# Performance work log

Hardware: AMD Instinct MI355X
Metric: run time of the kernel (lower is better)

## Reference

```python
import jax, jax.numpy as jnp
import numpy as np

N, E, D, H, L, NEF = 50000, 500000, 128, 4, 4, 7
Dh = D // H
LN_EPS = 1e-5


def layer_norm(x, g, b):
    mu = x.mean(-1, keepdims=True)
    var = ((x - mu) ** 2).mean(-1, keepdims=True)
    return (x - mu) / jnp.sqrt(var + LN_EPS) * g + b


def setup_inputs() -> dict:
    key = jax.random.key(0)
    ks = iter(jax.random.split(key, 64))
    p = lambda shape, s=0.05: jax.random.normal(next(ks), shape, dtype=jnp.float32) * s
    inp = {
        'x_nodes': jnp.zeros((N,), dtype=jnp.int32),
        'edge_index': jax.random.randint(next(ks), (2, E), 0, N, dtype=jnp.int32),
        'edge_attr': p((E, NEF), 1.0),
        'node_table': p((1, D), 1.0),
        'Wee': p((NEF, D)), 'bee': jnp.zeros((D,), jnp.float32),
        'Wq': p((L, D, D)), 'bq': jnp.zeros((L, D), jnp.float32),
        'Wk': p((L, D, D)), 'bk': jnp.zeros((L, D), jnp.float32),
        'Wv': p((L, D, D)), 'bv': jnp.zeros((L, D), jnp.float32),
        'We': p((L, D, D)), 'be': jnp.zeros((L, D), jnp.float32),
        'Ws': p((L, D, D)), 'bs': jnp.zeros((L, D), jnp.float32),
        'W1': p((L, D, 2 * D)), 'b1': jnp.zeros((L, 2 * D), jnp.float32),
        'W2': p((L, 2 * D, D)), 'b2': jnp.zeros((L, D), jnp.float32),
        'n1g': jnp.ones((L, D), jnp.float32), 'n1b': jnp.zeros((L, D), jnp.float32),
        'n2g': jnp.ones((L, D), jnp.float32), 'n2b': jnp.zeros((L, D), jnp.float32),
        'lng': jnp.ones((L, D), jnp.float32), 'lnb': jnp.zeros((L, D), jnp.float32),
    }
    return inp


def reference(x_nodes, edge_index, edge_attr, node_table, Wee, bee,
              Wq, bq, Wk, bk, Wv, bv, We, be, Ws, bs,
              W1, b1, W2, b2, n1g, n1b, n2g, n2b, lng, lnb):
    src, dst = edge_index[0], edge_index[1]
    scale = 1.0 / np.sqrt(Dh).astype(np.float32)
    # node encoder: Embedding(1, D) with indices clamped to [0, 0]
    h = node_table[jnp.clip(x_nodes, 0, 0)]              # [N, D]
    ee = edge_attr @ Wee + bee                            # [E, D]
    for l in range(L):
        h_in = h
        # TransformerConv (PyG semantics, root_weight=True, eval mode)
        q = (h_in @ Wq[l] + bq[l]).reshape(N, H, Dh)
        k = (h_in @ Wk[l] + bk[l]).reshape(N, H, Dh)
        v = (h_in @ Wv[l] + bv[l]).reshape(N, H, Dh)
        e = (ee @ We[l] + be[l]).reshape(E, H, Dh)
        ke = k[src] + e                                   # [E, H, Dh]
        ve = v[src] + e                                   # [E, H, Dh]
        alpha = (q[dst] * ke).sum(-1) * scale             # [E, H]
        m = jax.ops.segment_max(alpha, dst, num_segments=N)
        m = jnp.where(jnp.isfinite(m), m, 0.0)
        ex = jnp.exp(alpha - m[dst])
        den = jax.ops.segment_sum(ex, dst, num_segments=N) + 1e-16
        attn = ex / den[dst]                              # [E, H]
        agg = jax.ops.segment_sum(attn[:, :, None] * ve, dst, num_segments=N)
        att_out = agg.reshape(N, D) + (h_in @ Ws[l] + bs[l])  # skip (root) term
        # transformer block: residual + LN, FFN + residual + LN
        x1 = layer_norm(h_in + att_out, n1g[l], n1b[l])
        ff = jax.nn.leaky_relu(x1 @ W1[l] + b1[l]) @ W2[l] + b2[l]
        hconv = layer_norm(x1 + ff, n2g[l], n2b[l])
        # outer per-layer LayerNorm + activation (except last) + residual
        hn = layer_norm(hconv, lng[l], lnb[l])
        if l < L - 1:
            hn = jax.nn.leaky_relu(hn)
        h = hn + h_in
    return h  # JK == 'last'
```

## Files before the change

kernel.cpp:

```cpp
#include <hip/hip_runtime.h>
#include <hip/hip_bf16.h>
#include <math.h>

#define N_NODES 50000
#define N_EDGES 500000
#define DIM     128
#define NLAYER  4
#define NEFEAT  7

static constexpr float LN_EPS    = 1e-5f;
static constexpr float ATT_SCALE = 0.17677669529663687f;

typedef short s16x8 __attribute__((ext_vector_type(8)));
typedef float f32x4 __attribute__((ext_vector_type(4)));

static __device__ __forceinline__ float leaky(float x){ return x >= 0.f ? x : 0.01f*x; }

static __device__ __forceinline__ unsigned short f2bf(float f){
    __hip_bfloat16 b = __float2bfloat16(f);
    return *reinterpret_cast<unsigned short*>(&b);
}
static __device__ __forceinline__ float bflo(unsigned int u){ return __uint_as_float(u << 16); }
static __device__ __forceinline__ float bfhi(unsigned int u){ return __uint_as_float(u & 0xFFFF0000u); }

template<int CTRL>
static __device__ __forceinline__ float dpp_ror_add(float x){
    int r = __builtin_amdgcn_update_dpp(0, __float_as_int(x), CTRL, 0xf, 0xf, true);
    return x + __int_as_float(r);
}
static __device__ __forceinline__ float sum16(float x){
    x = dpp_ror_add<0x128>(x);
    x = dpp_ror_add<0x124>(x);
    x = dpp_ror_add<0x122>(x);
    x = dpp_ror_add<0x121>(x);
    return x;
}
static __device__ __forceinline__ float sum64(float x){
    x = sum16(x);
    x += __shfl_xor(x, 16);
    x += __shfl_xor(x, 32);
    return x;
}

__global__ void init_h_kernel(const float* __restrict__ node_table,
                              float* __restrict__ h, unsigned short* __restrict__ hb){
    int i = blockIdx.x*blockDim.x + threadIdx.x;
    if (i < N_NODES*DIM){
        float v = node_table[i & (DIM-1)];
        h[i]  = v;
        hb[i] = f2bf(v);
    }
}

__global__ void zero2_kernel(int* __restrict__ a, int* __restrict__ b){
    int i = blockIdx.x*blockDim.x + threadIdx.x;
    if (i < N_NODES){ a[i] = 0; b[i] = 0; }
}

__global__ void count_kernel(const int* __restrict__ dst, int* __restrict__ cnt){
    int e = blockIdx.x*blockDim.x + threadIdx.x;
    if (e < N_EDGES) atomicAdd(&cnt[dst[e]], 1);
}

__global__ void scan_kernel(const int* __restrict__ cnt, int* __restrict__ rowptr){
    __shared__ int wsum[16];
    __shared__ int runsh;
    if (threadIdx.x == 0) runsh = 0;
    __syncthreads();
    int lane = threadIdx.x & 63, wid = threadIdx.x >> 6;
    for (int base = 0; base < N_NODES; base += 1024){
        int i = base + (int)threadIdx.x;
        int vv = (i < N_NODES) ? cnt[i] : 0;
        int s = vv;
        #pragma unroll
        for (int off = 1; off < 64; off <<= 1){
            int t = __shfl_up(s, off);
            if (lane >= off) s += t;
        }
        if (lane == 63) wsum[wid] = s;
        __syncthreads();
        if (wid == 0 && lane < 16){
            int x = wsum[lane];
            #pragma unroll
            for (int off = 1; off < 16; off <<= 1){
                int t = __shfl_up(x, off);
                if (lane >= off) x += t;
            }
            wsum[lane] = x;
        }
        __syncthreads();
        int wpre = (wid == 0) ? 0 : wsum[wid-1];
        int run  = runsh;
        if (i < N_NODES) rowptr[i] = run + wpre + s - vv;
        __syncthreads();
        if (threadIdx.x == 0) runsh = run + wsum[15];
        __syncthreads();
    }
    if (threadIdx.x == 0) rowptr[N_NODES] = runsh;
}

__global__ void scatter_kernel(const int* __restrict__ src, const int* __restrict__ dst,
                               const float* __restrict__ edge_attr,
                               const int* __restrict__ rowptr, int* __restrict__ fill,
                               int* __restrict__ srcs, unsigned int* __restrict__ eab){
    int e = blockIdx.x*blockDim.x + threadIdx.x;
    if (e >= N_EDGES) return;
    int d   = dst[e];
    int pos = rowptr[d] + atomicAdd(&fill[d], 1);
    srcs[pos] = src[e];
    const float* a = edge_attr + (size_t)e*NEFEAT;
    uint4 u;
    u.x = (unsigned int)f2bf(a[0]) | ((unsigned int)f2bf(a[1]) << 16);
    u.y = (unsigned int)f2bf(a[2]) | ((unsigned int)f2bf(a[3]) << 16);
    u.z = (unsigned int)f2bf(a[4]) | ((unsigned int)f2bf(a[5]) << 16);
    u.w = (unsigned int)f2bf(a[6]) | (0x3F80u << 16);
    *(uint4*)(eab + (size_t)pos*4) = u;
}

__global__ void weff_all_kernel(const float* __restrict__ Wee, const float* __restrict__ bee,
                                const float* __restrict__ We, const float* __restrict__ be,
                                float* __restrict__ weff){
    int l = blockIdx.x;
    int d = threadIdx.x;
    const float* We_l = We + (size_t)l*DIM*DIM;
    float* out = weff + (size_t)l*8*DIM;
    for (int c = 0; c < NEFEAT; ++c){
        float s = 0.f;
        for (int t = 0; t < DIM; ++t) s += Wee[c*DIM + t] * We_l[t*DIM + d];
        out[c*DIM + d] = s;
    }
    float s = 0.f;
    for (int t = 0; t < DIM; ++t) s += bee[t] * We_l[t*DIM + d];
    out[7*DIM + d] = s + be[l*DIM + d];
}

__global__ void prepw_kernel(const float* __restrict__ Wq, const float* __restrict__ Wk,
                             const float* __restrict__ Wv, const float* __restrict__ Ws,
                             const float* __restrict__ W1, const float* __restrict__ W2,
                             unsigned short* __restrict__ wqkvsT,
                             unsigned short* __restrict__ w1T,
                             unsigned short* __restrict__ w2T){
    int tid = blockIdx.x*blockDim.x + threadIdx.x;
    if (tid >= NLAYER*131072) return;
    int l = tid >> 17;
    int r = tid & 131071;
    if (r < 65536){
        int n = r >> 7, k = r & 127;
        int p = n >> 7, nn = n & 127;
        const float* W = (p==0)?Wq:(p==1)?Wk:(p==2)?Wv:Ws;
        float val = W[(size_t)l*DIM*DIM + (size_t)k*DIM + nn];
        wqkvsT[(size_t)l*65536 + (size_t)n*128 + k] = f2bf(val);
    } else if (r < 98304){
        int r2 = r - 65536;
        int n = r2 >> 7, k = r2 & 127;
        float val = W1[(size_t)l*32768 + (size_t)k*256 + n];
        w1T[(size_t)l*32768 + (size_t)n*128 + k] = f2bf(val);
    } else {
        int r2 = r - 98304;
        int n = r2 >> 8, k = r2 & 255;
        float val = W2[(size_t)l*32768 + (size_t)k*128 + n];
        w2T[(size_t)l*32768 + (size_t)n*256 + k] = f2bf(val);
    }
}

__global__ __launch_bounds__(256) void qkvs_mfma_kernel(
    const unsigned short* __restrict__ hb, const unsigned short* __restrict__ wT,
    const float* __restrict__ bq, const float* __restrict__ bk,
    const float* __restrict__ bv, const float* __restrict__ bs,
    unsigned int* __restrict__ qs, unsigned int* __restrict__ kv)
{
    __shared__ char sA[32*256];
    int row0 = blockIdx.x*32;
    for (int idx = threadIdx.x; idx < 512; idx += 256){
        int row = idx >> 4, k16 = idx & 15;
        int byte = row*256 + k16*16;  byte ^= (row & 7) << 4;
        s16x8 val = {0,0,0,0,0,0,0,0};
        int grow = row0 + row;
        if (grow < N_NODES) val = *(const s16x8*)(hb + (size_t)grow*128 + k16*8);
        *(s16x8*)(sA + byte) = val;
    }
    __syncthreads();

    int w = threadIdx.x >> 6, l = threadIdx.x & 63;
    int y = blockIdx.y;
    int pb0 = y ? 128 : 0;
    int pb1 = y ? 256 : 384;

    f32x4 acc[2][4];
    #pragma unroll
    for (int rf=0;rf<2;++rf)
        #pragma unroll
        for (int cf=0;cf<4;++cf) acc[rf][cf] = (f32x4){0.f,0.f,0.f,0.f};

    s16x8 af[2][2], bf[2][4];
    #pragma unroll
    for (int rf=0;rf<2;++rf){
        int row = rf*16 + (l & 15);
        int byte = row*256 + (l >> 4)*16;  byte ^= (row & 7) << 4;
        af[0][rf] = *(const s16x8*)(sA + byte);
    }
    #pragma unroll
    for (int cf=0;cf<4;++cf){
        int nrow = ((cf < 2) ? pb0 : pb1) + (w<<5) + ((cf&1)<<4) + (l & 15);
        bf[0][cf] = *(const s16x8*)(wT + (size_t)nrow*128 + (l >> 4)*8);
    }
    #pragma unroll
    for (int kb = 0; kb < 4; ++kb){
        int cur = kb & 1, nxt = cur ^ 1;
        if (kb < 3){
            #pragma unroll
            for (int rf=0;rf<2;++rf){
                int row = rf*16 + (l & 15);
                int byte = row*256 + (kb+1)*64 + (l >> 4)*16;  byte ^= (row & 7) << 4;
                af[nxt][rf] = *(const s16x8*)(sA + byte);
            }
            #pragma unroll
            for (int cf=0;cf<4;++cf){
                int nrow = ((cf < 2) ? pb0 : pb1) + (w<<5) + ((cf&1)<<4) + (l & 15);
                bf[nxt][cf] = *(const s16x8*)(wT + (size_t)nrow*128 + (kb+1)*32 + (l >> 4)*8);
            }
        }
        #pragma unroll
        for (int rf=0;rf<2;++rf)
            #pragma unroll
            for (int cf=0;cf<4;++cf)
                acc[rf][cf] = __builtin_amdgcn_mfma_f32_16x16x32_bf16(af[cur][rf], bf[cur][cf], acc[rf][cf], 0, 0, 0);
    }

    const float* biasLo = y ? bk : bq;
    const float* biasHi = y ? bv : bs;
    unsigned int* outp  = y ? kv : qs;
    #pragma unroll
    for (int cp = 0; cp < 2; ++cp){
        int col = (w<<5) + (cp<<4) + (l & 15);
        float blo = biasLo[col], bhi = biasHi[col];
        #pragma unroll
        for (int rf=0;rf<2;++rf){
            #pragma unroll
            for (int r=0;r<4;++r){
                int row = row0 + rf*16 + ((l >> 4) << 2) + r;
                if (row < N_NODES){
                    float lo = acc[rf][cp][r]   + blo;
                    float hi = acc[rf][cp+2][r] + bhi;
                    outp[(size_t)row*128 + col] =
                        (unsigned int)f2bf(lo) | ((unsigned int)f2bf(hi) << 16);
                }
            }
        }
    }
}

__global__ __launch_bounds__(256) void attn_kernel(
    const unsigned int* __restrict__ qs, const unsigned int* __restrict__ kv,
    const float* __restrict__ weff_l, const int* __restrict__ rowptr,
    const int* __restrict__ srcs, const unsigned int* __restrict__ eab,
    const float* __restrict__ h,
    const float* __restrict__ n1g, const float* __restrict__ n1b,
    unsigned short* __restrict__ x1b)
{
    __shared__ float wf[8][DIM];
    __shared__ float els[4][64][9];
    for (int i = threadIdx.x; i < 8*DIM; i += 256) ((float*)wf)[i] = weff_l[i];
    __syncthreads();
    int wv = threadIdx.x >> 6, lane = threadIdx.x & 63;
    int n = blockIdx.x*4 + wv;
    if (n >= N_NODES) return;
    float (*el)[9] = els[wv];

    int d0 = lane*2;
    int fi = lane & 15;
    int fc = fi & 7;

    uint2 qsb = *(const uint2*)(qs + (size_t)n*DIM + d0);
    float q0 = bflo(qsb.x)*ATT_SCALE, q1 = bflo(qsb.y)*ATT_SCALE;
    float s0 = bfhi(qsb.x), s1 = bfhi(qsb.y);

    float qe[8];
    #pragma unroll
    for (int c = 0; c < 8; ++c){
        float2 wc = *(const float2*)&wf[c][d0];
        qe[c] = sum16(q0*wc.x + q1*wc.y);
    }
    float qaug = qe[0];
    qaug = (fc==1) ? qe[1] : qaug;
    qaug = (fc==2) ? qe[2] : qaug;
    qaug = (fc==3) ? qe[3] : qaug;
    qaug = (fc==4) ? qe[4] : qaug;
    qaug = (fc==5) ? qe[5] : qaug;
    qaug = (fc==6) ? qe[6] : qaug;
    qaug = (fc==7) ? qe[7] : qaug;
    qaug = (fi < 8) ? qaug : 0.f;

    int beg = rowptr[n], deg = rowptr[n+1] - beg;
    float a0 = 0.f, a1 = 0.f, peaL = 0.f;

    for (int cb = 0; cb < deg; cb += 64){
        int base = beg + cb;
        int cdeg = deg - cb; if (cdeg > 64) cdeg = 64;
        int srcv = 0;
        uint4 eu = {0u,0u,0u,0u};
        if (cb + lane < deg){
            srcv = srcs[base + lane];
            eu = *(const uint4*)(eab + ((size_t)(base + lane) << 2));
        }
        asm volatile("s_waitcnt lgkmcnt(0)" ::: "memory");
        __builtin_amdgcn_sched_barrier(0);
        {
            float* row = el[lane];
            row[0] = bflo(eu.x); row[1] = bfhi(eu.x);
            row[2] = bflo(eu.y); row[3] = bfhi(eu.y);
            row[4] = bflo(eu.z); row[5] = bfhi(eu.z);
            row[6] = bflo(eu.w); row[7] = bfhi(eu.w);
        }
        asm volatile("s_waitcnt lgkmcnt(0)" ::: "memory");
        __builtin_amdgcn_sched_barrier(0);

        int j = 0;
        for (; j + 1 < cdeg; j += 2){
            int svA = __builtin_amdgcn_readlane(srcv, j);
            int svB = __builtin_amdgcn_readlane(srcv, j+1);
            uint2 kvA = *(const uint2*)(kv + (size_t)svA*DIM + d0);
            uint2 kvB = *(const uint2*)(kv + (size_t)svB*DIM + d0);
            float eaA = el[j][fc];
            float eaB = el[j+1][fc];
            float pA = sum16(q0*bflo(kvA.x) + q1*bflo(kvA.y) + qaug*eaA);
            float pB = sum16(q0*bflo(kvB.x) + q1*bflo(kvB.y) + qaug*eaB);
            float ppA = __expf(pA);
            float ppB = __expf(pB);
            a0   += ppA*bfhi(kvA.x) + ppB*bfhi(kvB.x);
            a1   += ppA*bfhi(kvA.y) + ppB*bfhi(kvB.y);
            peaL += ppA*eaA + ppB*eaB;
        }
        if (j < cdeg){
            int sv = __builtin_amdgcn_readlane(srcv, j);
            uint2 kva = *(const uint2*)(kv + (size_t)sv*DIM + d0);
            float ea = el[j][fc];
            float p = sum16(q0*bflo(kva.x) + q1*bflo(kva.y) + qaug*ea);
            float pp = __expf(p);
            a0   += pp*bfhi(kva.x);
            a1   += pp*bfhi(kva.y);
            peaL += pp*ea;
        }
    }

    int hb_ = lane & 48;
    float pc0 = __shfl(peaL, hb_ + 0);
    float pc1 = __shfl(peaL, hb_ + 1);
    float pc2 = __shfl(peaL, hb_ + 2);
    float pc3 = __shfl(peaL, hb_ + 3);
    float pc4 = __shfl(peaL, hb_ + 4);
    float pc5 = __shfl(peaL, hb_ + 5);
    float pc6 = __shfl(peaL, hb_ + 6);
    float den = __shfl(peaL, hb_ + 7);

    float inv = (den > 0.f) ? 1.f/den : 0.f;
    float ev0, ev1;
    {
        float2 w0 = *(const float2*)&wf[0][d0];
        float2 w1c = *(const float2*)&wf[1][d0];
        float2 w2c = *(const float2*)&wf[2][d0];
        float2 w3c = *(const float2*)&wf[3][d0];
        float2 w4c = *(const float2*)&wf[4][d0];
        float2 w5c = *(const float2*)&wf[5][d0];
        float2 w6c = *(const float2*)&wf[6][d0];
        float2 w7c = *(const float2*)&wf[7][d0];
        ev0 = pc0*w0.x + pc1*w1c.x + pc2*w2c.x + pc3*w3c.x
            + pc4*w4c.x + pc5*w5c.x + pc6*w6c.x + den*w7c.x;
        ev1 = pc0*w0.y + pc1*w1c.y + pc2*w2c.y + pc3*w3c.y
            + pc4*w4c.y + pc5*w5c.y + pc6*w6c.y + den*w7c.y;
    }

    float2 hv = *(const float2*)(h + (size_t)n*DIM + d0);
    float t0 = hv.x + (a0 + ev0)*inv + s0;
    float t1 = hv.y + (a1 + ev1)*inv + s1;
    float sum = sum64(t0 + t1);
    float ss  = sum64(t0*t0 + t1*t1);
    float mu = sum * (1.f/DIM);
    float rstd = rsqrtf(ss*(1.f/DIM) - mu*mu + LN_EPS);
    float o0 = (t0-mu)*rstd*n1g[d0]   + n1b[d0];
    float o1 = (t1-mu)*rstd*n1g[d0+1] + n1b[d0+1];
    unsigned int pk = (unsigned int)f2bf(o0) | ((unsigned int)f2bf(o1) << 16);
    *(unsigned int*)(x1b + (size_t)n*DIM + d0) = pk;
}

__global__ __launch_bounds__(256) void ffn_mfma_kernel(
    const unsigned short* __restrict__ x1b,
    const float* __restrict__ hin,
    const unsigned short* __restrict__ w1T, const float* __restrict__ b1,
    const unsigned short* __restrict__ w2T, const float* __restrict__ b2,
    const float* __restrict__ n2g, const float* __restrict__ n2b,
    const float* __restrict__ lng, const float* __restrict__ lnb,
    int apply_act, float* __restrict__ h, unsigned short* __restrict__ hb)
{
    __shared__ char smem[24576];
    char* sA   = smem;
    char* sMid = smem + 8192;
    int row0 = blockIdx.x*32;
    for (int idx = threadIdx.x; idx < 512; idx += 256){
        int row = idx >> 4, k16 = idx & 15;
        int byte = row*256 + k16*16;  byte ^= (row & 7) << 4;
        s16x8 val = {0,0,0,0,0,0,0,0};
        int grow = row0 + row;
        if (grow < N_NODES) val = *(const s16x8*)(x1b + (size_t)grow*128 + k16*8);
        *(s16x8*)(sA + byte) = val;
    }
    __syncthreads();

    int w = threadIdx.x >> 6, l = threadIdx.x & 63;

    {
        int n0 = w*64;
        f32x4 acc[2][4];
        #pragma unroll
        for (int rf=0;rf<2;++rf)
            #pragma unroll
            for (int cf=0;cf<4;++cf) acc[rf][cf] = (f32x4){0.f,0.f,0.f,0.f};
        s16x8 af[2][2], bfr[2][4];
        #pragma unroll
        for (int rf=0;rf<2;++rf){
            int row = rf*16 + (l & 15);
            int byte = row*256 + (l >> 4)*16;  byte ^= (row & 7) << 4;
            af[0][rf] = *(const s16x8*)(sA + byte);
        }
        #pragma unroll
        for (int cf=0;cf<4;++cf){
            int n = n0 + cf*16 + (l & 15);
            bfr[0][cf] = *(const s16x8*)(w1T + (size_t)n*128 + (l >> 4)*8);
        }
        #pragma unroll
        for (int kb = 0; kb < 4; ++kb){
            int cur = kb & 1, nxt = cur ^ 1;
            if (kb < 3){
                #pragma unroll
                for (int rf=0;rf<2;++rf){
                    int row = rf*16 + (l & 15);
                    int byte = row*256 + (kb+1)*64 + (l >> 4)*16;  byte ^= (row & 7) << 4;
                    af[nxt][rf] = *(const s16x8*)(sA + byte);
                }
                #pragma unroll
                for (int cf=0;cf<4;++cf){
                    int n = n0 + cf*16 + (l & 15);
                    bfr[nxt][cf] = *(const s16x8*)(w1T + (size_t)n*128 + (kb+1)*32 + (l >> 4)*8);
                }
            }
            #pragma unroll
            for (int rf=0;rf<2;++rf)
                #pragma unroll
                for (int cf=0;cf<4;++cf)
                    acc[rf][cf] = __builtin_amdgcn_mfma_f32_16x16x32_bf16(af[cur][rf], bfr[cur][cf], acc[rf][cf], 0, 0, 0);
        }
        #pragma unroll
        for (int cf=0;cf<4;++cf){
            int col = n0 + cf*16 + (l & 15);
            float bb = b1[col];
            #pragma unroll
            for (int rf=0;rf<2;++rf){
                #pragma unroll
                for (int r=0;r<4;++r){
                    int row = rf*16 + ((l >> 4) << 2) + r;
                    float val = leaky(acc[rf][cf][r] + bb);
                    int byte = row*512 + col*2;  byte ^= (row & 7) << 4;
                    *(unsigned short*)(sMid + byte) = f2bf(val);
                }
            }
        }
    }
    __syncthreads();

    f32x4 acc2[2][2];
    {
        int n0 = w*32;
        #pragma unroll
        for (int cf=0;cf<2;++cf)
            #pragma unroll
            for (int rf=0;rf<2;++rf) acc2[cf][rf] = (f32x4){0.f,0.f,0.f,0.f};
        s16x8 af[2][2], bfr[2][2];
        #pragma unroll
        for (int rf=0;rf<2;++rf){
            int row = rf*16 + (l & 15);
            int byte = row*512 + (l >> 4)*16;  byte ^= (row & 7) << 4;
            af[0][rf] = *(const s16x8*)(sMid + byte);
        }
        #pragma unroll
        for (int cf=0;cf<2;++cf){
            int n = n0 + cf*16 + (l & 15);
            bfr[0][cf] = *(const s16x8*)(w2T + (size_t)n*256 + (l >> 4)*8);
        }
        #pragma unroll
        for (int kb = 0; kb < 8; ++kb){
            int cur = kb & 1, nxt = cur ^ 1;
            if (kb < 7){
                #pragma unroll
                for (int rf=0;rf<2;++rf){
                    int row = rf*16 + (l & 15);
                    int byte = row*512 + (kb+1)*64 + (l >> 4)*16;  byte ^= (row & 7) << 4;
                    af[nxt][rf] = *(const s16x8*)(sMid + byte);
                }
                #pragma unroll
                for (int cf=0;cf<2;++cf){
                    int n = n0 + cf*16 + (l & 15);
                    bfr[nxt][cf] = *(const s16x8*)(w2T + (size_t)n*256 + (kb+1)*32 + (l >> 4)*8);
                }
            }
            #pragma unroll
            for (int cf=0;cf<2;++cf)
                #pragma unroll
                for (int rf=0;rf<2;++rf)
                    acc2[cf][rf] = __builtin_amdgcn_mfma_f32_16x16x32_bf16(af[cur][rf], bfr[cur][cf], acc2[cf][rf], 0, 0, 0);
        }
    }
    __syncthreads();

    float* sFF = (float*)sMid;
    {
        int n0 = w*32;
        #pragma unroll
        for (int cf=0;cf<2;++cf){
            int col = n0 + cf*16 + (l & 15);
            float bb = b2[col];
            #pragma unroll
            for (int rf=0;rf<2;++rf){
                #pragma unroll
                for (int r=0;r<4;++r){
                    int row = rf*16 + ((l >> 4) << 2) + r;
                    int byte = row*512 + col*4;  byte ^= (row & 7) << 4;
                    *(float*)((char*)sFF + byte) = acc2[cf][rf][r] + bb;
                }
            }
        }
    }
    __syncthreads();

    int d0 = l*2;
    float g2a = n2g[d0], g2b = n2g[d0+1], be2a = n2b[d0], be2b = n2b[d0+1];
    float gla = lng[d0], glb = lng[d0+1], bla = lnb[d0], blb = lnb[d0+1];
    for (int i = 0; i < 8; ++i){
        int rr = w*8 + i;
        int grow = row0 + rr;
        if (grow >= N_NODES) break;
        int byte = rr*512 + d0*4;  byte ^= (rr & 7) << 4;
        float2 ff = *(float2*)((char*)sFF + byte);
        int byteA = rr*256 + d0*2;  byteA ^= (rr & 7) << 4;
        unsigned int xu = *(unsigned int*)(sA + byteA);
        float2 hr = *(const float2*)(hin + (size_t)grow*DIM + d0);
        float t0 = bflo(xu) + ff.x, t1 = bfhi(xu) + ff.y;
        float sum = sum64(t0 + t1);
        float ss  = sum64(t0*t0 + t1*t1);
        float mu = sum*(1.f/DIM);
        float rstd = rsqrtf(ss*(1.f/DIM) - mu*mu + LN_EPS);
        float c0 = (t0-mu)*rstd*g2a + be2a;
        float c1 = (t1-mu)*rstd*g2b + be2b;
        float sum2 = sum64(c0 + c1);
        float ss2  = sum64(c0*c0 + c1*c1);
        float mu2 = sum2*(1.f/DIM);
        float rstd2 = rsqrtf(ss2*(1.f/DIM) - mu2*mu2 + LN_EPS);
        float z0 = (c0-mu2)*rstd2*gla + bla;
        float z1 = (c1-mu2)*rstd2*glb + blb;
        if (apply_act){ z0 = leaky(z0); z1 = leaky(z1); }
        float o0 = z0 + hr.x, o1 = z1 + hr.y;
        *(float2*)(h + (size_t)grow*DIM + d0) = make_float2(o0, o1);
        unsigned int pk = (unsigned int)f2bf(o0) | ((unsigned int)f2bf(o1) << 16);
        *(unsigned int*)(hb + (size_t)grow*DIM + d0) = pk;
    }
}

extern "C" void kernel_launch(void* const* d_in, const int* in_sizes, int n_in,
                              void* d_out, int out_size, void* d_ws, size_t ws_size,
                              hipStream_t stream)
{
    const int*   edge_index = (const int*)  d_in[1];
    const float* edge_attr  = (const float*)d_in[2];
    const float* node_table = (const float*)d_in[3];
    const float* Wee = (const float*)d_in[4];
    const float* bee = (const float*)d_in[5];
    const float* Wq  = (const float*)d_in[6];  const float* bq = (const float*)d_in[7];
    const float* Wk  = (const float*)d_in[8];  const float* bk = (const float*)d_in[9];
    const float* Wv  = (const float*)d_in[10]; const float* bv = (const float*)d_in[11];
    const float* We  = (const float*)d_in[12]; const float* be = (const float*)d_in[13];
    const float* Ws  = (const float*)d_in[14]; const float* bs = (const float*)d_in[15];
    const float* W1  = (const float*)d_in[16]; const float* b1 = (const float*)d_in[17];
    const float* W2  = (const float*)d_in[18]; const float* b2 = (const float*)d_in[19];
    const float* n1g = (const float*)d_in[20]; const float* n1b = (const float*)d_in[21];
    const float* n2g = (const float*)d_in[22]; const float* n2b = (const float*)d_in[23];
    const float* lng = (const float*)d_in[24]; const float* lnb = (const float*)d_in[25];

    float* h = (float*)d_out;

    char* ws = (char*)d_ws;
    size_t off = 0;
    auto alloc = [&](size_t bytes)->void*{
        void* p = ws + off;
        off += (bytes + 255) & ~(size_t)255;
        return p;
    };
    unsigned int*   qs   = (unsigned int*)  alloc(sizeof(int)*(size_t)N_NODES*DIM);
    unsigned int*   kv   = (unsigned int*)  alloc(sizeof(int)*(size_t)N_NODES*DIM);
    unsigned short* hb   = (unsigned short*)alloc(sizeof(short)*(size_t)N_NODES*DIM);
    unsigned short* x1b  = (unsigned short*)alloc(sizeof(short)*(size_t)N_NODES*DIM);
    unsigned int*   eab  = (unsigned int*)  alloc(sizeof(int)*(size_t)N_EDGES*4);
    unsigned short* wqkvsT = (unsigned short*)alloc(sizeof(short)*NLAYER*512*128);
    unsigned short* w1T    = (unsigned short*)alloc(sizeof(short)*NLAYER*256*128);
    unsigned short* w2T    = (unsigned short*)alloc(sizeof(short)*NLAYER*128*256);
    float* weff = (float*)alloc(sizeof(float)*NLAYER*8*DIM);
    int* rowptr = (int*)alloc(sizeof(int)*(N_NODES+1));
    int* cnt    = (int*)alloc(sizeof(int)*N_NODES);
    int* fill   = (int*)alloc(sizeof(int)*N_NODES);
    int* srcs   = (int*)alloc(sizeof(int)*N_EDGES);

    const int* srcIdx = edge_index;
    const int* dstIdx = edge_index + N_EDGES;

    init_h_kernel<<<(N_NODES*DIM+255)/256, 256, 0, stream>>>(node_table, h, hb);
    zero2_kernel<<<(N_NODES+255)/256, 256, 0, stream>>>(cnt, fill);
    count_kernel<<<(N_EDGES+255)/256, 256, 0, stream>>>(dstIdx, cnt);
    scan_kernel<<<1, 1024, 0, stream>>>(cnt, rowptr);
    scatter_kernel<<<(N_EDGES+255)/256, 256, 0, stream>>>(srcIdx, dstIdx, edge_attr,
                                                          rowptr, fill, srcs, eab);
    prepw_kernel<<<(NLAYER*131072+255)/256, 256, 0, stream>>>(Wq, Wk, Wv, Ws, W1, W2,
                                                              wqkvsT, w1T, w2T);
    weff_all_kernel<<<NLAYER, 128, 0, stream>>>(Wee, bee, We, be, weff);

    int tiles32 = (N_NODES + 31)/32;
    for (int l = 0; l < NLAYER; ++l){
        qkvs_mfma_kernel<<<dim3(tiles32, 2), 256, 0, stream>>>(hb,
            wqkvsT + (size_t)l*65536,
            bq + (size_t)l*DIM, bk + (size_t)l*DIM, bv + (size_t)l*DIM, bs + (size_t)l*DIM,
            qs, kv);
        attn_kernel<<<(N_NODES+3)/4, 256, 0, stream>>>(qs, kv,
            weff + (size_t)l*8*DIM, rowptr, srcs, eab, h,
            n1g + (size_t)l*DIM, n1b + (size_t)l*DIM, x1b);
        ffn_mfma_kernel<<<tiles32, 256, 0, stream>>>(x1b, h,
            w1T + (size_t)l*32768, b1 + (size_t)l*2*DIM,
            w2T + (size_t)l*32768, b2 + (size_t)l*DIM,
            n2g + (size_t)l*DIM, n2b + (size_t)l*DIM,
            lng + (size_t)l*DIM, lnb + (size_t)l*DIM,
            (l < NLAYER-1) ? 1 : 0, h, hb);
    }
}
```

Measured before the change: 662.9 us.

## Fuse next-layer QKVS projection into FFN kernel and parallelize CSR scan

The FFN kernel now keeps the new bf16 hidden rows in shared memory and computes the next layer's Q/K/V/S projection directly, dropping the separate qkvs kernel launches and the hb round trip through global memory for layers after the first. The single-block serial prefix scan is replaced with a three-kernel block scan. Residual loads are hoisted ahead of the LayerNorm loop. In exchange, each FFN block does more work (64 output columns per wave, two passes), which adds register pressure, and the FFN grid has half as many blocks as the old 2D qkvs grid.

```diff
diff --git a/kernel.cpp b/kernel.cpp
--- a/kernel.cpp
+++ b/kernel.cpp
@@ -62,41 +62,53 @@
     if (e < N_EDGES) atomicAdd(&cnt[dst[e]], 1);
 }
 
-__global__ void scan_kernel(const int* __restrict__ cnt, int* __restrict__ rowptr){
+__global__ void scan1_kernel(const int* __restrict__ cnt, int* __restrict__ rowptr,
+                             int* __restrict__ bsum){
     __shared__ int wsum[16];
-    __shared__ int runsh;
-    if (threadIdx.x == 0) runsh = 0;
-    __syncthreads();
-    int lane = threadIdx.x & 63, wid = threadIdx.x >> 6;
-    for (int base = 0; base < N_NODES; base += 1024){
-        int i = base + (int)threadIdx.x;
-        int vv = (i < N_NODES) ? cnt[i] : 0;
-        int s = vv;
-        #pragma unroll
-        for (int off = 1; off < 64; off <<= 1){
-            int t = __shfl_up(s, off);
-            if (lane >= off) s += t;
-        }
-        if (lane == 63) wsum[wid] = s;
-        __syncthreads();
-        if (wid == 0 && lane < 16){
-            int x = wsum[lane];
-            #pragma unroll
-            for (int off = 1; off < 16; off <<= 1){
-                int t = __shfl_up(x, off);
-                if (lane >= off) x += t;
-            }
-            wsum[lane] = x;
-        }
-        __syncthreads();
-        int wpre = (wid == 0) ? 0 : wsum[wid-1];
-        int run  = runsh;
-        if (i < N_NODES) rowptr[i] = run + wpre + s - vv;
-        __syncthreads();
-        if (threadIdx.x == 0) runsh = run + wsum[15];
-        __syncthreads();
-    }
-    if (threadIdx.x == 0) rowptr[N_NODES] = runsh;
+    int t = threadIdx.x;
+    int i = blockIdx.x*1024 + t;
+    int lane = t & 63, wid = t >> 6;
+    int v = (i < N_NODES) ? cnt[i] : 0;
+    int s = v;
+    #pragma unroll
+    for (int off = 1; off < 64; off <<= 1){
+        int tt = __shfl_up(s, off);
+        if (lane >= off) s += tt;
+    }
+    if (lane == 63) wsum[wid] = s;
+    __syncthreads();
+    if (wid == 0 && lane < 16){
+        int x = wsum[lane];
+        #pragma unroll
+        for (int off = 1; off < 16; off <<= 1){
+            int tt = __shfl_up(x, off);
+            if (lane >= off) x += tt;
+        }
+        wsum[lane] = x;
+    }
+    __syncthreads();
+    int wpre = (wid == 0) ? 0 : wsum[wid-1];
+    if (i < N_NODES) rowptr[i] = wpre + s - v;
+    if (t == 1023) bsum[blockIdx.x] = wpre + s;
+}
+
+__global__ void scan2_kernel(const int* __restrict__ bsum, int* __restrict__ boff,
+                             int nb, int* __restrict__ totalp){
+    int t = threadIdx.x;
+    int v = (t < nb) ? bsum[t] : 0;
+    int s = v;
+    #pragma unroll
+    for (int off = 1; off < 64; off <<= 1){
+        int tt = __shfl_up(s, off);
+        if (t >= off) s += tt;
+    }
+    if (t < nb) boff[t] = s - v;
+    if (t == 63) *totalp = s;
+}
+
+__global__ void scan3_kernel(int* __restrict__ rowptr, const int* __restrict__ boff){
+    int i = blockIdx.x*1024 + threadIdx.x;
+    if (i < N_NODES) rowptr[i] += boff[blockIdx.x];
 }
 
 __global__ void scatter_kernel(const int* __restrict__ src, const int* __restrict__ dst,
@@ -383,14 +395,18 @@
     *(unsigned int*)(x1b + (size_t)n*DIM + d0) = pk;
 }
 
-__global__ __launch_bounds__(256) void ffn_mfma_kernel(
+__global__ __launch_bounds__(256) void ffn_qkvs_kernel(
     const unsigned short* __restrict__ x1b,
     const float* __restrict__ hin,
     const unsigned short* __restrict__ w1T, const float* __restrict__ b1,
     const unsigned short* __restrict__ w2T, const float* __restrict__ b2,
     const float* __restrict__ n2g, const float* __restrict__ n2b,
     const float* __restrict__ lng, const float* __restrict__ lnb,
-    int apply_act, float* __restrict__ h, unsigned short* __restrict__ hb)
+    int apply_act, float* __restrict__ h,
+    int do_qkvs, const unsigned short* __restrict__ wTn,
+    const float* __restrict__ bqn, const float* __restrict__ bkn,
+    const float* __restrict__ bvn, const float* __restrict__ bsn,
+    unsigned int* __restrict__ qs, unsigned int* __restrict__ kv)
 {
     __shared__ char smem[24576];
     char* sA   = smem;
@@ -534,6 +550,14 @@
     int d0 = l*2;
     float g2a = n2g[d0], g2b = n2g[d0+1], be2a = n2b[d0], be2b = n2b[d0+1];
     float gla = lng[d0], glb = lng[d0+1], bla = lnb[d0], blb = lnb[d0+1];
+    float2 hrv[8];
+    #pragma unroll
+    for (int i = 0; i < 8; ++i){
+        int grow = row0 + w*8 + i;
+        hrv[i] = make_float2(0.f, 0.f);
+        if (grow < N_NODES) hrv[i] = *(const float2*)(hin + (size_t)grow*DIM + d0);
+    }
+    #pragma unroll
     for (int i = 0; i < 8; ++i){
         int rr = w*8 + i;
         int grow = row0 + rr;
@@ -542,7 +566,6 @@
         float2 ff = *(float2*)((char*)sFF + byte);
         int byteA = rr*256 + d0*2;  byteA ^= (rr & 7) << 4;
         unsigned int xu = *(unsigned int*)(sA + byteA);
-        float2 hr = *(const float2*)(hin + (size_t)grow*DIM + d0);
         float t0 = bflo(xu) + ff.x, t1 = bfhi(xu) + ff.y;
         float sum = sum64(t0 + t1);
         float ss  = sum64(t0*t0 + t1*t1);
@@ -557,10 +580,79 @@
         float z0 = (c0-mu2)*rstd2*gla + bla;
         float z1 = (c1-mu2)*rstd2*glb + blb;
         if (apply_act){ z0 = leaky(z0); z1 = leaky(z1); }
-        float o0 = z0 + hr.x, o1 = z1 + hr.y;
+        float o0 = z0 + hrv[i].x, o1 = z1 + hrv[i].y;
         *(float2*)(h + (size_t)grow*DIM + d0) = make_float2(o0, o1);
         unsigned int pk = (unsigned int)f2bf(o0) | ((unsigned int)f2bf(o1) << 16);
-        *(unsigned int*)(hb + (size_t)grow*DIM + d0) = pk;
+        *(unsigned int*)(sA + byteA) = pk;
+    }
+
+    if (!do_qkvs) return;
+    __syncthreads();
+
+    #pragma unroll
+    for (int y = 0; y < 2; ++y){
+        int pb0 = y ? 128 : 0;
+        int pb1 = y ? 256 : 384;
+        f32x4 acc[2][4];
+        #pragma unroll
+        for (int rf=0;rf<2;++rf)
+            #pragma unroll
+            for (int cf=0;cf<4;++cf) acc[rf][cf] = (f32x4){0.f,0.f,0.f,0.f};
+        s16x8 af[2][2], bf[2][4];
+        #pragma unroll
+        for (int rf=0;rf<2;++rf){
+            int row = rf*16 + (l & 15);
+            int byte = row*256 + (l >> 4)*16;  byte ^= (row & 7) << 4;
+            af[0][rf] = *(const s16x8*)(sA + byte);
+        }
+        #pragma unroll
+        for (int cf=0;cf<4;++cf){
+            int nrow = ((cf < 2) ? pb0 : pb1) + (w<<5) + ((cf&1)<<4) + (l & 15);
+            bf[0][cf] = *(const s16x8*)(wTn + (size_t)nrow*128 + (l >> 4)*8);
+        }
+        #pragma unroll
+        for (int kb = 0; kb < 4; ++kb){
+            int cur = kb & 1, nxt = cur ^ 1;
+            if (kb < 3){
+                #pragma unroll
+                for (int rf=0;rf<2;++rf){
+                    int row = rf*16 + (l & 15);
+                    int byte = row*256 + (kb+1)*64 + (l >> 4)*16;  byte ^= (row & 7) << 4;
+                    af[nxt][rf] = *(const s16x8*)(sA + byte);
+                }
+                #pragma unroll
+                for (int cf=0;cf<4;++cf){
+                    int nrow = ((cf < 2) ? pb0 : pb1) + (w<<5) + ((cf&1)<<4) + (l & 15);
+                    bf[nxt][cf] = *(const s16x8*)(wTn + (size_t)nrow*128 + (kb+1)*32 + (l >> 4)*8);
+                }
+            }
+            #pragma unroll
+            for (int rf=0;rf<2;++rf)
+                #pragma unroll
+                for (int cf=0;cf<4;++cf)
+                    acc[rf][cf] = __builtin_amdgcn_mfma_f32_16x16x32_bf16(af[cur][rf], bf[cur][cf], acc[rf][cf], 0, 0, 0);
+        }
+        const float* biasLo = y ? bkn : bqn;
+        const float* biasHi = y ? bvn : bsn;
+        unsigned int* outp  = y ? kv : qs;
+        #pragma unroll
+        for (int cp = 0; cp < 2; ++cp){
+            int col = (w<<5) + (cp<<4) + (l & 15);
+            float blo = biasLo[col], bhi = biasHi[col];
+            #pragma unroll
+            for (int rf=0;rf<2;++rf){
+                #pragma unroll
+                for (int r=0;r<4;++r){
+                    int row = row0 + rf*16 + ((l >> 4) << 2) + r;
+                    if (row < N_NODES){
+                        float lo = acc[rf][cp][r]   + blo;
+                        float hi = acc[rf][cp+2][r] + bhi;
+                        outp[(size_t)row*128 + col] =
+                            (unsigned int)f2bf(lo) | ((unsigned int)f2bf(hi) << 16);
+                    }
+                }
+            }
+        }
     }
 }
 
@@ -606,14 +698,19 @@
     int* cnt    = (int*)alloc(sizeof(int)*N_NODES);
     int* fill   = (int*)alloc(sizeof(int)*N_NODES);
     int* srcs   = (int*)alloc(sizeof(int)*N_EDGES);
+    int* bsum   = (int*)alloc(sizeof(int)*64);
+    int* boff   = (int*)alloc(sizeof(int)*64);
 
     const int* srcIdx = edge_index;
     const int* dstIdx = edge_index + N_EDGES;
+    int nb = (N_NODES + 1023)/1024;
 
     init_h_kernel<<<(N_NODES*DIM+255)/256, 256, 0, stream>>>(node_table, h, hb);
     zero2_kernel<<<(N_NODES+255)/256, 256, 0, stream>>>(cnt, fill);
     count_kernel<<<(N_EDGES+255)/256, 256, 0, stream>>>(dstIdx, cnt);
-    scan_kernel<<<1, 1024, 0, stream>>>(cnt, rowptr);
+    scan1_kernel<<<nb, 1024, 0, stream>>>(cnt, rowptr, bsum);
+    scan2_kernel<<<1, 64, 0, stream>>>(bsum, boff, nb, rowptr + N_NODES);
+    scan3_kernel<<<nb, 1024, 0, stream>>>(rowptr, boff);
     scatter_kernel<<<(N_EDGES+255)/256, 256, 0, stream>>>(srcIdx, dstIdx, edge_attr,
                                                           rowptr, fill, srcs, eab);
     prepw_kernel<<<(NLAYER*131072+255)/256, 256, 0, stream>>>(Wq, Wk, Wv, Ws, W1, W2,
@@ -621,19 +718,24 @@
     weff_all_kernel<<<NLAYER, 128, 0, stream>>>(Wee, bee, We, be, weff);
 
     int tiles32 = (N_NODES + 31)/32;
+    qkvs_mfma_kernel<<<dim3(tiles32, 2), 256, 0, stream>>>(hb, wqkvsT,
+        bq, bk, bv, bs, qs, kv);
     for (int l = 0; l < NLAYER; ++l){
-        qkvs_mfma_kernel<<<dim3(tiles32, 2), 256, 0, stream>>>(hb,
-            wqkvsT + (size_t)l*65536,
-            bq + (size_t)l*DIM, bk + (size_t)l*DIM, bv + (size_t)l*DIM, bs + (size_t)l*DIM,
-            qs, kv);
         attn_kernel<<<(N_NODES+3)/4, 256, 0, stream>>>(qs, kv,
             weff + (size_t)l*8*DIM, rowptr, srcs, eab, h,
             n1g + (size_t)l*DIM, n1b + (size_t)l*DIM, x1b);
-        ffn_mfma_kernel<<<tiles32, 256, 0, stream>>>(x1b, h,
+        int has = (l < NLAYER-1);
+        ffn_qkvs_kernel<<<tiles32, 256, 0, stream>>>(x1b, h,
             w1T + (size_t)l*32768, b1 + (size_t)l*2*DIM,
             w2T + (size_t)l*32768, b2 + (size_t)l*DIM,
             n2g + (size_t)l*DIM, n2b + (size_t)l*DIM,
             lng + (size_t)l*DIM, lnb + (size_t)l*DIM,
-            (l < NLAYER-1) ? 1 : 0, h, hb);
-    }
-}
+            has, h,
+            has, wqkvsT + (size_t)(l+1 < NLAYER ? l+1 : 0)*65536,
+            bq + (size_t)(l+1 < NLAYER ? l+1 : 0)*DIM,
+            bk + (size_t)(l+1 < NLAYER ? l+1 : 0)*DIM,
+            bv + (size_t)(l+1 < NLAYER ? l+1 : 0)*DIM,
+            bs + (size_t)(l+1 < NLAYER ? l+1 : 0)*DIM,
+            qs, kv);
+    }
+}
```

New measurement: 581.9 us. 1.14x faster.
